# Kernel optimization log

Hardware: AMD Instinct MI355X
Metric: run time of the kernel (lower is better)

## Reference

```python
import jax, jax.numpy as jnp
import numpy as np

N_NODES = 50000
N_EDGES = 800000
HID = 256
HEADS = 4
HEAD_C = HID // HEADS  # 64
IN_CH = 16
OUT_CH = 4
NEG_SLOPE = 0.2  # PyG GATConv default LeakyReLU slope
LN_EPS = 1e-5


def setup_inputs() -> dict:
    key = jax.random.key(0)
    ks = jax.random.split(key, 12)
    s = 0.05
    return {
        "x": jax.random.normal(ks[0], (N_NODES, IN_CH), dtype=jnp.float32),
        "edge_index": jax.random.randint(ks[1], (2, N_EDGES), 0, N_NODES, dtype=jnp.int64),
        "w_in": jax.random.normal(ks[2], (IN_CH, HID), dtype=jnp.float32) * s,
        "b_in": jnp.zeros((HID,), dtype=jnp.float32),
        "w_gat": jax.random.normal(ks[3], (4, HID, HID), dtype=jnp.float32) * s,
        "att_src": jax.random.normal(ks[4], (4, HEADS, HEAD_C), dtype=jnp.float32) * s,
        "att_dst": jax.random.normal(ks[5], (4, HEADS, HEAD_C), dtype=jnp.float32) * s,
        "b_gat": jnp.zeros((4, HID), dtype=jnp.float32),
        "ln_scale": jnp.ones((4, HID), dtype=jnp.float32),
        "ln_bias": jnp.zeros((4, HID), dtype=jnp.float32),
        "w_out": jax.random.normal(ks[6], (HID, OUT_CH), dtype=jnp.float32) * s,
        "b_out": jnp.zeros((OUT_CH,), dtype=jnp.float32),
    }


def _gat_layer(x, src, dst, W, a_src, a_dst, bias, g, beta):
    """One GATConv(concat, heads=4) + LayerNorm + ELU. x:[N,HID]."""
    n = x.shape[0]
    h = (x @ W).reshape(n, HEADS, HEAD_C)                 # [N,H,C]
    a_s = jnp.einsum("nhc,hc->nh", h, a_src)              # [N,H]
    a_d = jnp.einsum("nhc,hc->nh", h, a_dst)              # [N,H]
    logits = jax.nn.leaky_relu(a_s[src] + a_d[dst], NEG_SLOPE)  # [E,H]
    # segment softmax over destination neighborhoods (self-loops ensure non-empty)
    m = jax.ops.segment_max(logits, dst, num_segments=n)
    e = jnp.exp(logits - m[dst])
    denom = jax.ops.segment_sum(e, dst, num_segments=n)
    alpha = e / (denom[dst] + 1e-16)                      # [E,H]
    msg = alpha[:, :, None] * h[src]                      # [E,H,C]
    out = jax.ops.segment_sum(msg, dst, num_segments=n).reshape(n, HID) + bias
    mu = out.mean(-1, keepdims=True)
    var = out.var(-1, keepdims=True)
    out = (out - mu) * jax.lax.rsqrt(var + LN_EPS) * g + beta
    return jax.nn.elu(out)


def reference(x, edge_index, w_in, b_in, w_gat, att_src, att_dst, b_gat,
              ln_scale, ln_bias, w_out, b_out):
    n = x.shape[0]
    # PyG GATConv adds self-loops by default
    loops = jnp.arange(n, dtype=edge_index.dtype)
    ei = jnp.concatenate([edge_index, jnp.stack([loops, loops])], axis=1)
    src, dst = ei[0], ei[1]

    x = x @ w_in + b_in                                   # input_proj
    h = x
    for l in (0, 1):
        h = _gat_layer(h, src, dst, w_gat[l], att_src[l], att_dst[l],
                       b_gat[l], ln_scale[l], ln_bias[l])
    x = x + h
    h = x
    for l in (2, 3):
        h = _gat_layer(h, src, dst, w_gat[l], att_src[l], att_dst[l],
                       b_gat[l], ln_scale[l], ln_bias[l])
    x = x + h
    return x @ w_out + b_out
```

## Files before the change

kernel.cpp:

```cpp
#include <hip/hip_runtime.h>
#include <math.h>

#define NN 50000
#define E0 800000
#define ET 850000
#define HID 256
#define INCH 16
#define MAXDEG 64

#define NB_P1   416
#define EPB     2048
#define NBUCK   196

#define NB_WT   256
#define NB_IP   6250
#define NB_PREP (NB_P1 + NB_WT + NB_IP)

#define NB_G    782
#define NB_G0   (NBUCK + NB_G)

typedef _Float16 h8 __attribute__((ext_vector_type(8)));
typedef _Float16 h4 __attribute__((ext_vector_type(4)));
typedef float f32x4 __attribute__((ext_vector_type(4)));

__device__ __forceinline__ void load_lds16(const void* g, void* l) {
    __builtin_amdgcn_global_load_lds(
        (const __attribute__((address_space(1))) unsigned int*)g,
        (__attribute__((address_space(3))) unsigned int*)l, 16, 0, 0);
}

__global__ __launch_bounds__(256) void prep_kernel(
    const float* __restrict__ w_gat, _Float16* __restrict__ WT,
    const float* __restrict__ x, const float* __restrict__ w_in,
    const float* __restrict__ b_in, _Float16* __restrict__ Ph,
    const int* __restrict__ ei, unsigned int* __restrict__ pairs,
    int* __restrict__ cnt_g, int* __restrict__ off_g) {
    __shared__ unsigned int hist[256], pref[256], cur2[256];
    int b = blockIdx.x, t = threadIdx.x;
    if (b < NB_P1) {
        hist[t] = 0;
        __syncthreads();
        unsigned int pk[8];
        int base = b * EPB + t;
#pragma unroll
        for (int k = 0; k < 8; ++k) {
            int e = base + k * 256;
            pk[k] = 0xFFFFFFFFu;
            if (e < ET) {
                int s, d;
                if (e < E0) { s = ei[e]; d = ei[E0 + e]; }
                else        { s = d = e - E0; }
                pk[k] = ((unsigned int)d << 16) | (unsigned int)s;
                atomicAdd(&hist[d >> 8], 1u);
            }
        }
        __syncthreads();
        unsigned int h = hist[t];
        pref[t] = h;
        __syncthreads();
#pragma unroll
        for (int o = 1; o < 256; o <<= 1) {
            unsigned int v = (t >= o) ? pref[t - o] : 0u;
            __syncthreads();
            pref[t] += v;
            __syncthreads();
        }
        unsigned int ex = pref[t] - h;
        cur2[t] = ex;
        if (t < NBUCK) {
            cnt_g[b * NBUCK + t] = (int)h;
            off_g[b * NBUCK + t] = (int)ex;
        }
        __syncthreads();
#pragma unroll
        for (int k = 0; k < 8; ++k) {
            if (pk[k] != 0xFFFFFFFFu) {
                unsigned int g = pk[k] >> 24;
                unsigned int pos = atomicAdd(&cur2[g], 1u);
                pairs[b * EPB + pos] = pk[k];
            }
        }
    } else if (b < NB_P1 + NB_WT) {
        int k = b - NB_P1;
#pragma unroll
        for (int l = 0; l < 4; ++l) {
            float v = w_gat[((size_t)l * 256 + k) * 256 + t];
            WT[((size_t)l * 256 + t) * 256 + k] = (_Float16)v;
        }
    } else {
        int ipb = b - NB_P1 - NB_WT;
        int sub = t >> 5, l32 = t & 31;
        int n = ipb * 8 + sub;
        int c0 = l32 * 8;
        const float* xr = x + n * INCH;
        float a[8];
#pragma unroll
        for (int k = 0; k < 8; k += 4) {
            float4 bb = *(const float4*)(b_in + c0 + k);
            a[k] = bb.x; a[k + 1] = bb.y; a[k + 2] = bb.z; a[k + 3] = bb.w;
        }
#pragma unroll
        for (int k = 0; k < INCH; ++k) {
            float xv = xr[k];
            const float4 w0 = *(const float4*)(w_in + k * 256 + c0);
            const float4 w1 = *(const float4*)(w_in + k * 256 + c0 + 4);
            a[0] += xv * w0.x; a[1] += xv * w0.y; a[2] += xv * w0.z; a[3] += xv * w0.w;
            a[4] += xv * w1.x; a[5] += xv * w1.y; a[6] += xv * w1.z; a[7] += xv * w1.w;
        }
        h8 o;
#pragma unroll
        for (int k = 0; k < 8; ++k) o[k] = (_Float16)a[k];
        *(h8*)(Ph + (size_t)n * 256 + c0) = o;
    }
}

__device__ __forceinline__ void gemm_tile(
    int rb, int cb,
    const _Float16* __restrict__ A, const _Float16* __restrict__ BT,
    _Float16* __restrict__ H, const float* __restrict__ att_s,
    const float* __restrict__ att_d, float* __restrict__ AS, float* __restrict__ AD,
    _Float16* As, _Float16* Bs) {
    int t = threadIdx.x;
    int wv = t >> 6, lane = t & 63;
    int wr = (wv >> 1) * 64, wc = (wv & 1) * 64;
    int lm = lane & 15, lq = lane >> 4;
    f32x4 acc[4][4] = {};

    int rch = lane >> 2;
    int q = lane & 3;

    for (int k0 = 0; k0 < 256; k0 += 32) {
#pragma unroll
        for (int c = 0; c < 2; ++c) {
            int r = wv * 32 + c * 16 + rch;
            int g = q ^ (r & 3);
            int ra = rb + r; if (ra >= NN) ra = NN - 1;
            load_lds16(A + (size_t)ra * 256 + k0 + g * 8,
                       (char*)As + wv * 2048 + c * 1024);
            load_lds16(BT + (size_t)(cb + r) * 256 + k0 + g * 8,
                       (char*)Bs + wv * 2048 + c * 1024);
        }
        __syncthreads();
        h8 af[4], bfr[4];
#pragma unroll
        for (int i = 0; i < 4; ++i) {
            int row = wr + i * 16 + lm;
            af[i] = *(const h8*)((const char*)As + row * 64 + ((lq ^ (row & 3)) * 16));
        }
#pragma unroll
        for (int j = 0; j < 4; ++j) {
            int row = wc + j * 16 + lm;
            bfr[j] = *(const h8*)((const char*)Bs + row * 64 + ((lq ^ (row & 3)) * 16));
        }
#pragma unroll
        for (int i = 0; i < 4; ++i)
#pragma unroll
            for (int j = 0; j < 4; ++j)
                acc[i][j] = __builtin_amdgcn_mfma_f32_16x16x32_f16(af[i], bfr[j], acc[i][j], 0, 0, 0);
        __syncthreads();
    }

    int head = (cb + wc) >> 6;
    float sa[4], sd[4];
#pragma unroll
    for (int j = 0; j < 4; ++j) {
        sa[j] = att_s[head * 64 + j * 16 + lm];
        sd[j] = att_d[head * 64 + j * 16 + lm];
    }
#pragma unroll
    for (int i = 0; i < 4; ++i)
#pragma unroll
        for (int rr = 0; rr < 4; ++rr) {
            float vs = acc[i][0][rr] * sa[0] + acc[i][1][rr] * sa[1]
                     + acc[i][2][rr] * sa[2] + acc[i][3][rr] * sa[3];
            float vd = acc[i][0][rr] * sd[0] + acc[i][1][rr] * sd[1]
                     + acc[i][2][rr] * sd[2] + acc[i][3][rr] * sd[3];
#pragma unroll
            for (int o = 1; o <= 8; o <<= 1) {
                vs += __shfl_xor(vs, o, 64);
                vd += __shfl_xor(vd, o, 64);
            }
            int row = rb + wr + i * 16 + lq * 4 + rr;
            if (lm == 0 && row < NN) {
                AS[row * 4 + head] = vs;
                AD[row * 4 + head] = vd;
            }
        }

#pragma unroll
    for (int i = 0; i < 4; ++i)
#pragma unroll
        for (int j = 0; j < 4; ++j) {
            int col = cb + wc + j * 16 + lm;
#pragma unroll
            for (int rr = 0; rr < 4; ++rr) {
                int row = rb + wr + i * 16 + lq * 4 + rr;
                if (row < NN) H[(size_t)row * 256 + col] = (_Float16)acc[i][j][rr];
            }
        }
}

__global__ __launch_bounds__(256) void gemm_fused_kernel(
    const _Float16* __restrict__ A, const _Float16* __restrict__ BT,
    _Float16* __restrict__ H, const float* __restrict__ att_s,
    const float* __restrict__ att_d, float* __restrict__ AS, float* __restrict__ AD) {
    __shared__ _Float16 As[128 * 32];
    __shared__ _Float16 Bs[128 * 32];
    gemm_tile(blockIdx.x * 128, blockIdx.y * 128, A, BT, H, att_s, att_d, AS, AD, As, Bs);
}

__global__ __launch_bounds__(256) void gemm0_p2_kernel(
    const _Float16* __restrict__ A, const _Float16* __restrict__ BT,
    _Float16* __restrict__ H, const float* __restrict__ att_s,
    const float* __restrict__ att_d, float* __restrict__ AS, float* __restrict__ AD,
    const unsigned int* __restrict__ pairs, const int* __restrict__ cnt_g,
    const int* __restrict__ off_g, int* __restrict__ cursor,
    unsigned short* __restrict__ csr_pad) {
    __shared__ _Float16 As[128 * 32];
    __shared__ _Float16 Bs[128 * 32];
    int b = blockIdx.x;
    if (b < NBUCK) {
        int g = b, t = threadIdx.x;
        unsigned int* curs = (unsigned int*)As;
        curs[t] = 0;
        __syncthreads();
        for (int sb = t; sb < NB_P1; sb += 256) {
            int c = cnt_g[sb * NBUCK + g];
            int o = off_g[sb * NBUCK + g];
            const unsigned int* p = pairs + sb * EPB + o;
            for (int i = 0; i < c; ++i) {
                unsigned int pk = p[i];
                int d = (int)(pk >> 16);
                unsigned int pos = atomicAdd(&curs[d & 255], 1u);
                if (pos < MAXDEG)
                    csr_pad[((size_t)d << 6) + pos] = (unsigned short)(pk & 0xFFFFu);
            }
        }
        __syncthreads();
        int n = (g << 8) + t;
        if (n < NN) cursor[n] = (int)curs[t];
        return;
    }
    int g2 = b - NBUCK;
    gemm_tile((g2 >> 1) * 128, (g2 & 1) * 128, A, BT, H, att_s, att_d, AS, AD, As, Bs);
}

__global__ __launch_bounds__(256) void agg_kernel(
    const _Float16* __restrict__ H, const float4* __restrict__ AS,
    const float4* __restrict__ AD,
    const int* __restrict__ cnt, const unsigned short* __restrict__ csr_pad,
    const float* __restrict__ bias, const float* __restrict__ g, const float* __restrict__ beta,
    const _Float16* __restrict__ res, _Float16* __restrict__ outh,
    const float* __restrict__ wout, const float* __restrict__ bout,
    float* __restrict__ out) {
    __shared__ float eLs[4][256];
    __shared__ int   sLs[4][64];
    int t = threadIdx.x;
    int wv = t >> 6, lane = t & 63;
    int n = blockIdx.x * 4 + wv;
    int head = lane >> 4;
    int c0 = lane * 4;
    float* eL = eLs[wv];
    int*   sL = sLs[wv];

    int deg = cnt[n];
    if (deg > MAXDEG) deg = MAXDEG;
    float4 adv = AD[n];

    float4 e4 = make_float4(0.f, 0.f, 0.f, 0.f);
    int sv = 0;
    if (lane < deg) {
        sv = csr_pad[(n << 6) + lane];
        float4 as = AS[sv];
        float v0 = as.x + adv.x; v0 = (v0 >= 0.f) ? v0 : 0.2f * v0;
        float v1 = as.y + adv.y; v1 = (v1 >= 0.f) ? v1 : 0.2f * v1;
        float v2 = as.z + adv.z; v2 = (v2 >= 0.f) ? v2 : 0.2f * v2;
        float v3 = as.w + adv.w; v3 = (v3 >= 0.f) ? v3 : 0.2f * v3;
        e4 = make_float4(__expf(v0), __expf(v1), __expf(v2), __expf(v3));
    }
    sL[lane] = sv;
    *(float4*)(eL + c0) = e4;

    float acc0 = 0.f, acc1 = 0.f, acc2 = 0.f, acc3 = 0.f, acc_e = 0.f;
#pragma unroll 4
    for (int i = 0; i < deg; ++i) {
        float e = eL[i * 4 + head];
        int s = sL[i];
        h4 hv = *(const h4*)(H + (size_t)s * 256 + c0);
        acc_e += e;
        acc0 += e * (float)hv[0];
        acc1 += e * (float)hv[1];
        acc2 += e * (float)hv[2];
        acc3 += e * (float)hv[3];
    }
    float dinv = 1.f / (acc_e + 1e-16f);

    float4 bb = *(const float4*)(bias + c0);
    float val0 = acc0 * dinv + bb.x;
    float val1 = acc1 * dinv + bb.y;
    float val2 = acc2 * dinv + bb.z;
    float val3 = acc3 * dinv + bb.w;

    float s1 = val0 + val1 + val2 + val3;
    float s2 = val0 * val0 + val1 * val1 + val2 * val2 + val3 * val3;
#pragma unroll
    for (int o = 32; o >= 1; o >>= 1) {
        s1 += __shfl_xor(s1, o, 64);
        s2 += __shfl_xor(s2, o, 64);
    }
    float mu = s1 * (1.f / 256.f);
    float var = s2 * (1.f / 256.f) - mu * mu;
    float rs = rsqrtf(var + 1e-5f);

    float4 g4 = *(const float4*)(g + c0);
    float4 b4 = *(const float4*)(beta + c0);
    float y0 = (val0 - mu) * rs * g4.x + b4.x;
    float y1 = (val1 - mu) * rs * g4.y + b4.y;
    float y2 = (val2 - mu) * rs * g4.z + b4.z;
    float y3 = (val3 - mu) * rs * g4.w + b4.w;
    y0 = (y0 > 0.f) ? y0 : (__expf(y0) - 1.f);
    y1 = (y1 > 0.f) ? y1 : (__expf(y1) - 1.f);
    y2 = (y2 > 0.f) ? y2 : (__expf(y2) - 1.f);
    y3 = (y3 > 0.f) ? y3 : (__expf(y3) - 1.f);
    if (res) {
        h4 r0 = *(const h4*)(res + (size_t)n * 256 + c0);
        y0 += (float)r0[0]; y1 += (float)r0[1]; y2 += (float)r0[2]; y3 += (float)r0[3];
    }
    if (wout) {
        float4 w0 = *(const float4*)(wout + (size_t)(c0 + 0) * 4);
        float4 w1 = *(const float4*)(wout + (size_t)(c0 + 1) * 4);
        float4 w2 = *(const float4*)(wout + (size_t)(c0 + 2) * 4);
        float4 w3 = *(const float4*)(wout + (size_t)(c0 + 3) * 4);
        float o0 = y0 * w0.x + y1 * w1.x + y2 * w2.x + y3 * w3.x;
        float o1 = y0 * w0.y + y1 * w1.y + y2 * w2.y + y3 * w3.y;
        float o2 = y0 * w0.z + y1 * w1.z + y2 * w2.z + y3 * w3.z;
        float o3 = y0 * w0.w + y1 * w1.w + y2 * w2.w + y3 * w3.w;
#pragma unroll
        for (int o = 32; o >= 1; o >>= 1) {
            o0 += __shfl_xor(o0, o, 64);
            o1 += __shfl_xor(o1, o, 64);
            o2 += __shfl_xor(o2, o, 64);
            o3 += __shfl_xor(o3, o, 64);
        }
        if (lane == 0) {
            float4 ov = make_float4(o0 + bout[0], o1 + bout[1], o2 + bout[2], o3 + bout[3]);
            *(float4*)(out + (size_t)n * 4) = ov;
        }
    } else {
        h4 o0;
        o0[0] = (_Float16)y0; o0[1] = (_Float16)y1;
        o0[2] = (_Float16)y2; o0[3] = (_Float16)y3;
        *(h4*)(outh + (size_t)n * 256 + c0) = o0;
    }
}

extern "C" void kernel_launch(void* const* d_in, const int* in_sizes, int n_in,
                              void* d_out, int out_size, void* d_ws, size_t ws_size,
                              hipStream_t stream) {
    const float* x       = (const float*)d_in[0];
    const int*   ei      = (const int*)  d_in[1];
    const float* w_in    = (const float*)d_in[2];
    const float* b_in    = (const float*)d_in[3];
    const float* w_gat   = (const float*)d_in[4];
    const float* att_src = (const float*)d_in[5];
    const float* att_dst = (const float*)d_in[6];
    const float* b_gat   = (const float*)d_in[7];
    const float* ln_g    = (const float*)d_in[8];
    const float* ln_b    = (const float*)d_in[9];
    const float* w_out   = (const float*)d_in[10];
    const float* b_out   = (const float*)d_in[11];
    float* out = (float*)d_out;

    char* ws = (char*)d_ws;
    size_t off = 0;
    auto alloc = [&](size_t bytes) {
        void* p = ws + off;
        off += (bytes + 255) & ~(size_t)255;
        return p;
    };
    _Float16*       Ph      = (_Float16*)alloc((size_t)NN * HID * 2);
    _Float16*       Ch      = (_Float16*)alloc((size_t)NN * HID * 2);
    _Float16*       Gh      = (_Float16*)alloc((size_t)NN * HID * 2);
    _Float16*       H       = (_Float16*)alloc((size_t)NN * HID * 2);
    _Float16*       WT      = (_Float16*)alloc((size_t)4 * HID * HID * 2);
    float*          ASAD    = (float*)alloc((size_t)NN * 8 * 4);
    int*            cursor  = (int*)alloc((size_t)NN * 4);
    unsigned short* csr_pad = (unsigned short*)alloc((size_t)NN * MAXDEG * 2);
    unsigned int*   pairs   = (unsigned int*)alloc((size_t)NB_P1 * EPB * 4);
    int*            cnt_g   = (int*)alloc((size_t)NB_P1 * NBUCK * 4);
    int*            off_g   = (int*)alloc((size_t)NB_P1 * NBUCK * 4);

    float* AS = ASAD;
    float* AD = ASAD + (size_t)NN * 4;

    const dim3 GEMM_GRID(391, 2);
    const int NB_AGG = NN / 4;

    prep_kernel<<<NB_PREP, 256, 0, stream>>>(w_gat, WT, x, w_in, b_in, Ph,
                                             ei, pairs, cnt_g, off_g);

    gemm0_p2_kernel<<<NB_G0, 256, 0, stream>>>(
        Ph, WT, H, att_src, att_dst, AS, AD, pairs, cnt_g, off_g, cursor, csr_pad);
    agg_kernel<<<NB_AGG, 256, 0, stream>>>(
        H, (const float4*)AS, (const float4*)AD, cursor, csr_pad,
        b_gat, ln_g, ln_b, nullptr, Gh, nullptr, nullptr, nullptr);

    auto run_layer = [&](const _Float16* inh, int l, const _Float16* res, _Float16* outh,
                         const float* wo, const float* bo) {
        gemm_fused_kernel<<<GEMM_GRID, 256, 0, stream>>>(
            inh, WT + (size_t)l * HID * HID, H,
            att_src + l * 256, att_dst + l * 256, AS, AD);
        agg_kernel<<<NB_AGG, 256, 0, stream>>>(
            H, (const float4*)AS, (const float4*)AD, cursor, csr_pad,
            b_gat + l * 256, ln_g + l * 256, ln_b + l * 256, res, outh, wo, bo,
            wo ? out : nullptr);
    };

    run_layer(Gh, 1, Ph,      Ch, nullptr, nullptr);
    run_layer(Ch, 2, nullptr, Gh, nullptr, nullptr);
    run_layer(Gh, 3, Ch,      Ph, w_out,   b_out);
}
```

Before: 511.1 us.

## Double-buffer GEMM LDS staging, remap tile order, unroll aggregation loop deeper

```diff
diff --git a/kernel.cpp b/kernel.cpp
--- a/kernel.cpp
+++ b/kernel.cpp
@@ -16,7 +16,7 @@
 #define NB_IP   6250
 #define NB_PREP (NB_P1 + NB_WT + NB_IP)
 
-#define NB_G    782
+#define NB_G    784
 #define NB_G0   (NBUCK + NB_G)
 
 typedef _Float16 h8 __attribute__((ext_vector_type(8)));
@@ -129,28 +129,34 @@
     int rch = lane >> 2;
     int q = lane & 3;
 
-    for (int k0 = 0; k0 < 256; k0 += 32) {
+    auto stage = [&](int k0, int buf) {
 #pragma unroll
         for (int c = 0; c < 2; ++c) {
             int r = wv * 32 + c * 16 + rch;
             int g = q ^ (r & 3);
             int ra = rb + r; if (ra >= NN) ra = NN - 1;
             load_lds16(A + (size_t)ra * 256 + k0 + g * 8,
-                       (char*)As + wv * 2048 + c * 1024);
+                       (char*)As + buf * 8192 + wv * 2048 + c * 1024);
             load_lds16(BT + (size_t)(cb + r) * 256 + k0 + g * 8,
-                       (char*)Bs + wv * 2048 + c * 1024);
-        }
-        __syncthreads();
+                       (char*)Bs + buf * 8192 + wv * 2048 + c * 1024);
+        }
+    };
+
+    stage(0, 0);
+    __syncthreads();
+    int cur = 0;
+    for (int k0 = 0; k0 < 256; k0 += 32) {
+        if (k0 + 32 < 256) stage(k0 + 32, cur ^ 1);
         h8 af[4], bfr[4];
 #pragma unroll
         for (int i = 0; i < 4; ++i) {
             int row = wr + i * 16 + lm;
-            af[i] = *(const h8*)((const char*)As + row * 64 + ((lq ^ (row & 3)) * 16));
+            af[i] = *(const h8*)((const char*)As + cur * 8192 + row * 64 + ((lq ^ (row & 3)) * 16));
         }
 #pragma unroll
         for (int j = 0; j < 4; ++j) {
             int row = wc + j * 16 + lm;
-            bfr[j] = *(const h8*)((const char*)Bs + row * 64 + ((lq ^ (row & 3)) * 16));
+            bfr[j] = *(const h8*)((const char*)Bs + cur * 8192 + row * 64 + ((lq ^ (row & 3)) * 16));
         }
 #pragma unroll
         for (int i = 0; i < 4; ++i)
@@ -158,6 +164,7 @@
             for (int j = 0; j < 4; ++j)
                 acc[i][j] = __builtin_amdgcn_mfma_f32_16x16x32_f16(af[i], bfr[j], acc[i][j], 0, 0, 0);
         __syncthreads();
+        cur ^= 1;
     }
 
     int head = (cb + wc) >> 6;
@@ -200,13 +207,23 @@
         }
 }
 
+__device__ __forceinline__ bool gemm_map(int b, int& rb, int& cb) {
+    int r = (b >> 4) * 8 + (b & 7);
+    int h = (b >> 3) & 1;
+    if (r >= 391) return false;
+    rb = r * 128; cb = h * 128;
+    return true;
+}
+
 __global__ __launch_bounds__(256) void gemm_fused_kernel(
     const _Float16* __restrict__ A, const _Float16* __restrict__ BT,
     _Float16* __restrict__ H, const float* __restrict__ att_s,
     const float* __restrict__ att_d, float* __restrict__ AS, float* __restrict__ AD) {
-    __shared__ _Float16 As[128 * 32];
-    __shared__ _Float16 Bs[128 * 32];
-    gemm_tile(blockIdx.x * 128, blockIdx.y * 128, A, BT, H, att_s, att_d, AS, AD, As, Bs);
+    __shared__ _Float16 As[2 * 128 * 32];
+    __shared__ _Float16 Bs[2 * 128 * 32];
+    int rb, cb;
+    if (!gemm_map(blockIdx.x, rb, cb)) return;
+    gemm_tile(rb, cb, A, BT, H, att_s, att_d, AS, AD, As, Bs);
 }
 
 __global__ __launch_bounds__(256) void gemm0_p2_kernel(
@@ -216,8 +233,8 @@
     const unsigned int* __restrict__ pairs, const int* __restrict__ cnt_g,
     const int* __restrict__ off_g, int* __restrict__ cursor,
     unsigned short* __restrict__ csr_pad) {
-    __shared__ _Float16 As[128 * 32];
-    __shared__ _Float16 Bs[128 * 32];
+    __shared__ _Float16 As[2 * 128 * 32];
+    __shared__ _Float16 Bs[2 * 128 * 32];
     int b = blockIdx.x;
     if (b < NBUCK) {
         int g = b, t = threadIdx.x;
@@ -241,8 +258,9 @@
         if (n < NN) cursor[n] = (int)curs[t];
         return;
     }
-    int g2 = b - NBUCK;
-    gemm_tile((g2 >> 1) * 128, (g2 & 1) * 128, A, BT, H, att_s, att_d, AS, AD, As, Bs);
+    int rb, cb;
+    if (!gemm_map(b - NBUCK, rb, cb)) return;
+    gemm_tile(rb, cb, A, BT, H, att_s, att_d, AS, AD, As, Bs);
 }
 
 __global__ __launch_bounds__(256) void agg_kernel(
@@ -282,7 +300,7 @@
     *(float4*)(eL + c0) = e4;
 
     float acc0 = 0.f, acc1 = 0.f, acc2 = 0.f, acc3 = 0.f, acc_e = 0.f;
-#pragma unroll 4
+#pragma unroll 8
     for (int i = 0; i < deg; ++i) {
         float e = eL[i * 4 + head];
         int s = sL[i];
@@ -393,7 +411,6 @@
     float* AS = ASAD;
     float* AD = ASAD + (size_t)NN * 4;
 
-    const dim3 GEMM_GRID(391, 2);
     const int NB_AGG = NN / 4;
 
     prep_kernel<<<NB_PREP, 256, 0, stream>>>(w_gat, WT, x, w_in, b_in, Ph,
@@ -407,7 +424,7 @@
 
     auto run_layer = [&](const _Float16* inh, int l, const _Float16* res, _Float16* outh,
                          const float* wo, const float* bo) {
-        gemm_fused_kernel<<<GEMM_GRID, 256, 0, stream>>>(
+        gemm_fused_kernel<<<NB_G, 256, 0, stream>>>(
             inh, WT + (size_t)l * HID * HID, H,
             att_src + l * 256, att_dst + l * 256, AS, AD);
         agg_kernel<<<NB_AGG, 256, 0, stream>>>(
```

New measurement: 506.5 us. No clear change (-0.9%).
